# Optimization experiments

Hardware: AMD Instinct MI355X
Metric: run time of the kernel (lower is better)

## Reference

```python
import jax, jax.numpy as jnp
import numpy as np

B, H, W, C = 4, 64, 64, 512
D = C // 8  # query/key channels

def setup_inputs() -> dict:
    key = jax.random.key(0)
    k1, k2, k3, k4, k5 = jax.random.split(key, 5)
    x = jax.random.normal(k1, (B, H, W, C), dtype=jnp.float32)
    # 1x1 convs without bias == per-pixel matmuls; he_normal-ish scaling
    Wq = jax.random.normal(k2, (C, D), dtype=jnp.float32) * np.sqrt(2.0 / C)
    Wk = jax.random.normal(k3, (C, D), dtype=jnp.float32) * np.sqrt(2.0 / C)
    Wv = jax.random.normal(k4, (C, C), dtype=jnp.float32) * np.sqrt(2.0 / C)
    # original init is zeros; use small nonzero so the attention path is exercised
    gamma = jax.random.normal(k5, (1,), dtype=jnp.float32) * 0.1
    return {"x": x, "Wq": Wq, "Wk": Wk, "Wv": Wv, "gamma": gamma}

def reference(x, Wq, Wk, Wv, gamma):
    b, h, w, c = x.shape
    n = h * w
    xf = x.reshape(b, n, c)                      # flatten spatial dims
    q = xf @ Wq                                  # [b, n, c//8]
    k = xf @ Wk                                  # [b, n, c//8]
    v = xf @ Wv                                  # [b, n, c]
    scores = jnp.einsum('bnd,bmd->bnm', q, k)    # [b, n, n]
    attn = jax.nn.sigmoid(scores)                # activation_func='sigmoid' (no row normalization)
    attended = jnp.einsum('bnm,bmc->bnc', attn, v).reshape(b, h, w, c)
    return gamma * attended + x
```

## Files before the change

### kernel.cpp

```cpp
#include <hip/hip_runtime.h>

typedef short bf16x8 __attribute__((ext_vector_type(8)));
typedef float f32x4 __attribute__((ext_vector_type(4)));
typedef unsigned short ushort8v __attribute__((ext_vector_type(8)));
typedef unsigned short ushort4v __attribute__((ext_vector_type(4)));

__device__ __forceinline__ unsigned short f2bf(float f) {
  unsigned u = __float_as_uint(f);
  u += 0x7FFF + ((u >> 16) & 1);
  return (unsigned short)(u >> 16);
}

__global__ void wt_prep(const float* __restrict__ Wq, const float* __restrict__ Wk,
                        const float* __restrict__ Wv, unsigned short* __restrict__ WbT) {
  int idx = blockIdx.x * 256 + threadIdx.x;
  int o = idx >> 9, c = idx & 511;
  float v;
  if (o < 64)       v = Wq[c * 64 + o] * 1.44269504f;
  else if (o < 128) v = Wk[c * 64 + (o - 64)];
  else              v = Wv[(size_t)c * 512 + (o - 128)];
  WbT[idx] = f2bf(v);
}

__global__ __launch_bounds__(256, 2) void proj_gemm(
    const float* __restrict__ x, const unsigned short* __restrict__ WbT,
    unsigned short* __restrict__ q, unsigned short* __restrict__ k,
    unsigned short* __restrict__ vT) {
  __shared__ unsigned short As[128][72];
  const int tid = threadIdx.x;
  const int wid = tid >> 6, lane = tid & 63;
  const int l15 = lane & 15, l4 = lane >> 4;
  const int mtile = blockIdx.x, ntile = blockIdx.y;
  const int rbase = mtile * 128;
  const int wr = (wid >> 1) * 64, wc = (wid & 1) * 64;

  f32x4 acc[4][4] = {};

  const int arow = tid >> 2;
  const int akof = (tid & 3) * 16;

  for (int kb = 0; kb < 512; kb += 64) {
    f32x4 t0[2][4];
#pragma unroll
    for (int pass = 0; pass < 2; ++pass) {
      const float* src = x + (size_t)(rbase + pass * 64 + arow) * 512 + kb + akof;
#pragma unroll
      for (int i = 0; i < 4; ++i) t0[pass][i] = *(const f32x4*)(src + i * 4);
    }
    __syncthreads();
#pragma unroll
    for (int pass = 0; pass < 2; ++pass) {
      unsigned short tmp[16];
#pragma unroll
      for (int i = 0; i < 4; ++i)
#pragma unroll
        for (int j = 0; j < 4; ++j) tmp[i * 4 + j] = f2bf(t0[pass][i][j]);
      unsigned short* dst = &As[pass * 64 + arow][akof];
      *(ushort8v*)(dst)     = *(ushort8v*)(tmp);
      *(ushort8v*)(dst + 8) = *(ushort8v*)(tmp + 8);
    }
    __syncthreads();

    bf16x8 af[4][2], bfr[4][2];
#pragma unroll
    for (int mr = 0; mr < 4; ++mr)
#pragma unroll
      for (int ks = 0; ks < 2; ++ks)
        af[mr][ks] = *(const bf16x8*)&As[wr + mr * 16 + l15][ks * 32 + l4 * 8];
#pragma unroll
    for (int nc = 0; nc < 4; ++nc)
#pragma unroll
      for (int ks = 0; ks < 2; ++ks) {
        int col = ntile * 128 + wc + nc * 16 + l15;
        bfr[nc][ks] = *(const bf16x8*)(WbT + (size_t)col * 512 + kb + ks * 32 + l4 * 8);
      }
#pragma unroll
    for (int ks = 0; ks < 2; ++ks)
#pragma unroll
      for (int mr = 0; mr < 4; ++mr)
#pragma unroll
        for (int nc = 0; nc < 4; ++nc)
          acc[mr][nc] = __builtin_amdgcn_mfma_f32_16x16x32_bf16(af[mr][ks], bfr[nc][ks],
                                                                acc[mr][nc], 0, 0, 0);
  }

  if (ntile == 0) {
    unsigned short* dst = (wid & 1) ? k : q;
#pragma unroll
    for (int mr = 0; mr < 4; ++mr)
#pragma unroll
      for (int nc = 0; nc < 4; ++nc)
#pragma unroll
        for (int r = 0; r < 4; ++r) {
          int grow = rbase + wr + mr * 16 + l4 * 4 + r;
          int col = nc * 16 + l15;
          dst[(size_t)grow * 64 + col] = f2bf(acc[mr][nc][r]);
        }
  } else {
#pragma unroll
    for (int mr = 0; mr < 4; ++mr)
#pragma unroll
      for (int nc = 0; nc < 4; ++nc) {
        int col = ntile * 128 + wc + nc * 16 + l15 - 128;
        int grow = rbase + wr + mr * 16 + l4 * 4;
        int b = grow >> 12, m = grow & 4095;
        ushort4v pk;
#pragma unroll
        for (int r = 0; r < 4; ++r) pk[r] = f2bf(acc[mr][nc][r]);
        *(ushort4v*)(vT + ((size_t)b * 512 + col) * 4096 + m) = pk;
      }
  }
}

__global__ __launch_bounds__(512, 1) void attn_fused(
    const float* __restrict__ x, const unsigned short* __restrict__ q,
    const unsigned short* __restrict__ k, const unsigned short* __restrict__ vT,
    const float* __restrict__ gamma, float* __restrict__ out) {
  __shared__ unsigned short Vs[2][16][8][16][8];
  __shared__ unsigned short Ps[2][8][8][16][8];
  const int tid = threadIdx.x, w = tid >> 6, lane = tid & 63;
  const int l15 = lane & 15, l4 = lane >> 4;
  const int rhalf = w >> 2;
  const int mt = w & 3;
  const int pvt = w >> 1;
  const int ms = w & 1;
  const int rt = blockIdx.x, ct = blockIdx.y, b = blockIdx.z;
  const int rbase = rt * 128, cbase = ct * 256;
  const unsigned short* qb = q + (size_t)b * 4096 * 64;
  const unsigned short* kp = k + (size_t)b * 4096 * 64;
  const unsigned short* vb = vT + (size_t)b * 512 * 4096;
  const float gv = gamma[0];
  const int vst_c = tid >> 1, vhalf = tid & 1;

  bf16x8 qf[4][2];
#pragma unroll
  for (int rf = 0; rf < 4; ++rf)
#pragma unroll
    for (int ks = 0; ks < 2; ++ks)
      qf[rf][ks] = *(const bf16x8*)(qb +
          (size_t)(rbase + rhalf * 64 + rf * 16 + l15) * 64 + ks * 32 + l4 * 8);

  bf16x8 kfc[2];
#pragma unroll
  for (int ks = 0; ks < 2; ++ks)
    kfc[ks] = *(const bf16x8*)(kp + (size_t)(mt * 16 + l15) * 64 + ks * 32 + l4 * 8);
  {
    bf16x8 vv[4];
#pragma unroll
    for (int i = 0; i < 4; ++i)
      vv[i] = *(const bf16x8*)(vb + (size_t)(cbase + vst_c) * 4096 + vhalf * 32 + i * 8);
#pragma unroll
    for (int i = 0; i < 4; ++i)
      *(bf16x8*)&Vs[0][vst_c >> 4][vhalf * 4 + i][vst_c & 15][0] = vv[i];
  }

  f32x4 oacc[8][4] = {};

  for (int it = 0; it < 64; ++it) {
    const int mb_n = (it + 1) * 64;
    const bool pf = (it < 63);
    const int p = it & 1;
    bf16x8 kfn[2], vv[4];
    if (pf) {
#pragma unroll
      for (int ks = 0; ks < 2; ++ks)
        kfn[ks] = *(const bf16x8*)(kp + (size_t)(mb_n + mt * 16 + l15) * 64 + ks * 32 + l4 * 8);
#pragma unroll
      for (int i = 0; i < 4; ++i)
        vv[i] = *(const bf16x8*)(vb + (size_t)(cbase + vst_c) * 4096 + mb_n + vhalf * 32 + i * 8);
    }

    f32x4 sacc[4] = {};
#pragma unroll
    for (int ks = 0; ks < 2; ++ks)
#pragma unroll
      for (int rf = 0; rf < 4; ++rf)
        sacc[rf] = __builtin_amdgcn_mfma_f32_16x16x32_bf16(kfc[ks], qf[rf][ks], sacc[rf], 0, 0, 0);

#pragma unroll
    for (int rf = 0; rf < 4; ++rf) {
      ushort4v pk;
#pragma unroll
      for (int r = 0; r < 4; ++r) {
        float s = sacc[rf][r];
        pk[r] = f2bf(__builtin_amdgcn_rcpf(1.0f + __builtin_amdgcn_exp2f(-s)));
      }
      *(ushort4v*)&Ps[p][rhalf * 4 + rf][mt * 2 + (l4 >> 1)][l15][(l4 & 1) * 4] = pk;
    }
    __syncthreads();

    __builtin_amdgcn_s_setprio(1);
    {
      bf16x8 af[8], bfr[4];
#pragma unroll
      for (int mr = 0; mr < 8; ++mr)
        af[mr] = *(const bf16x8*)&Ps[p][mr][ms * 4 + l4][l15][0];
#pragma unroll
      for (int nc = 0; nc < 4; ++nc)
        bfr[nc] = *(const bf16x8*)&Vs[p][pvt * 4 + nc][ms * 4 + l4][l15][0];
#pragma unroll
      for (int mr = 0; mr < 8; ++mr)
#pragma unroll
        for (int nc = 0; nc < 4; ++nc)
          oacc[mr][nc] = __builtin_amdgcn_mfma_f32_16x16x32_bf16(af[mr], bfr[nc],
                                                                 oacc[mr][nc], 0, 0, 0);
    }
    __builtin_amdgcn_s_setprio(0);

    if (pf) {
#pragma unroll
      for (int i = 0; i < 4; ++i)
        *(bf16x8*)&Vs[p ^ 1][vst_c >> 4][vhalf * 4 + i][vst_c & 15][0] = vv[i];
      kfc[0] = kfn[0]; kfc[1] = kfn[1];
    }
  }

  float* red = (float*)&Vs[0][0][0][0][0];
  __syncthreads();
#pragma unroll
  for (int h = 0; h < 2; ++h) {
    if (ms == 1) {
#pragma unroll
      for (int m4 = 0; m4 < 4; ++m4)
#pragma unroll
        for (int nc = 0; nc < 4; ++nc)
#pragma unroll
          for (int r = 0; r < 4; ++r)
            red[(pvt * 64 + m4 * 16 + l4 * 4 + r) * 64 + nc * 16 + l15] =
                oacc[h * 4 + m4][nc][r];
    }
    __syncthreads();
    if (ms == 0) {
#pragma unroll
      for (int m4 = 0; m4 < 4; ++m4)
#pragma unroll
        for (int nc = 0; nc < 4; ++nc)
#pragma unroll
          for (int r = 0; r < 4; ++r) {
            int mr = h * 4 + m4;
            float sum = oacc[mr][nc][r] +
                red[(pvt * 64 + m4 * 16 + l4 * 4 + r) * 64 + nc * 16 + l15];
            int grow = rbase + mr * 16 + l4 * 4 + r;
            int col = cbase + pvt * 64 + nc * 16 + l15;
            size_t idx = ((size_t)b * 4096 + grow) * 512 + col;
            out[idx] = gv * sum + x[idx];
          }
    }
    __syncthreads();
  }
}

extern "C" void kernel_launch(void* const* d_in, const int* in_sizes, int n_in,
                              void* d_out, int out_size, void* d_ws, size_t ws_size,
                              hipStream_t stream) {
  const float* x     = (const float*)d_in[0];
  const float* Wq    = (const float*)d_in[1];
  const float* Wk    = (const float*)d_in[2];
  const float* Wv    = (const float*)d_in[3];
  const float* gamma = (const float*)d_in[4];
  float* out = (float*)d_out;

  char* ws = (char*)d_ws;
  unsigned short* qbuf = (unsigned short*)(ws);
  unsigned short* kbuf = (unsigned short*)(ws + (2ull << 20));
  unsigned short* vT   = (unsigned short*)(ws + (4ull << 20));
  unsigned short* WbT  = (unsigned short*)(ws + (20ull << 20));

  hipLaunchKernelGGL(wt_prep, dim3(1280), dim3(256), 0, stream, Wq, Wk, Wv, WbT);
  hipLaunchKernelGGL(proj_gemm, dim3(128, 5), dim3(256), 0, stream, x, WbT, qbuf, kbuf, vT);
  hipLaunchKernelGGL(attn_fused, dim3(32, 2, 4), dim3(512), 0, stream,
                     x, qbuf, kbuf, vT, gamma, out);
}
```

Before: 142.2 us.

## Software-pipeline QK scores one tile ahead of the PV matmul

```diff
diff --git a/kernel.cpp b/kernel.cpp
--- a/kernel.cpp
+++ b/kernel.cpp
@@ -140,10 +140,6 @@
       qf[rf][ks] = *(const bf16x8*)(qb +
           (size_t)(rbase + rhalf * 64 + rf * 16 + l15) * 64 + ks * 32 + l4 * 8);
 
-  bf16x8 kfc[2];
-#pragma unroll
-  for (int ks = 0; ks < 2; ++ks)
-    kfc[ks] = *(const bf16x8*)(kp + (size_t)(mt * 16 + l15) * 64 + ks * 32 + l4 * 8);
   {
     bf16x8 vv[4];
 #pragma unroll
@@ -152,42 +148,57 @@
 #pragma unroll
     for (int i = 0; i < 4; ++i)
       *(bf16x8*)&Vs[0][vst_c >> 4][vhalf * 4 + i][vst_c & 15][0] = vv[i];
-  }
+
+    bf16x8 k0[2];
+#pragma unroll
+    for (int ks = 0; ks < 2; ++ks)
+      k0[ks] = *(const bf16x8*)(kp + (size_t)(mt * 16 + l15) * 64 + ks * 32 + l4 * 8);
+    f32x4 s0[4] = {};
+#pragma unroll
+    for (int ks = 0; ks < 2; ++ks)
+#pragma unroll
+      for (int rf = 0; rf < 4; ++rf)
+        s0[rf] = __builtin_amdgcn_mfma_f32_16x16x32_bf16(k0[ks], qf[rf][ks], s0[rf], 0, 0, 0);
+#pragma unroll
+    for (int rf = 0; rf < 4; ++rf) {
+      ushort4v pk;
+#pragma unroll
+      for (int r = 0; r < 4; ++r)
+        pk[r] = f2bf(__builtin_amdgcn_rcpf(1.0f + __builtin_amdgcn_exp2f(-s0[rf][r])));
+      *(ushort4v*)&Ps[0][rhalf * 4 + rf][mt * 2 + (l4 >> 1)][l15][(l4 & 1) * 4] = pk;
+    }
+  }
+  bf16x8 kfc[2];
+#pragma unroll
+  for (int ks = 0; ks < 2; ++ks)
+    kfc[ks] = *(const bf16x8*)(kp + (size_t)(64 + mt * 16 + l15) * 64 + ks * 32 + l4 * 8);
+  __syncthreads();
 
   f32x4 oacc[8][4] = {};
 
   for (int it = 0; it < 64; ++it) {
-    const int mb_n = (it + 1) * 64;
     const bool pf = (it < 63);
     const int p = it & 1;
+    const int kn = (it + 2 < 64) ? (it + 2) : 63;
     bf16x8 kfn[2], vv[4];
+    f32x4 sacc[4] = {};
+
     if (pf) {
 #pragma unroll
+      for (int i = 0; i < 4; ++i)
+        vv[i] = *(const bf16x8*)(vb + (size_t)(cbase + vst_c) * 4096 +
+                                 (it + 1) * 64 + vhalf * 32 + i * 8);
+#pragma unroll
       for (int ks = 0; ks < 2; ++ks)
-        kfn[ks] = *(const bf16x8*)(kp + (size_t)(mb_n + mt * 16 + l15) * 64 + ks * 32 + l4 * 8);
-#pragma unroll
-      for (int i = 0; i < 4; ++i)
-        vv[i] = *(const bf16x8*)(vb + (size_t)(cbase + vst_c) * 4096 + mb_n + vhalf * 32 + i * 8);
-    }
-
-    f32x4 sacc[4] = {};
-#pragma unroll
-    for (int ks = 0; ks < 2; ++ks)
-#pragma unroll
-      for (int rf = 0; rf < 4; ++rf)
-        sacc[rf] = __builtin_amdgcn_mfma_f32_16x16x32_bf16(kfc[ks], qf[rf][ks], sacc[rf], 0, 0, 0);
-
-#pragma unroll
-    for (int rf = 0; rf < 4; ++rf) {
-      ushort4v pk;
-#pragma unroll
-      for (int r = 0; r < 4; ++r) {
-        float s = sacc[rf][r];
-        pk[r] = f2bf(__builtin_amdgcn_rcpf(1.0f + __builtin_amdgcn_exp2f(-s)));
-      }
-      *(ushort4v*)&Ps[p][rhalf * 4 + rf][mt * 2 + (l4 >> 1)][l15][(l4 & 1) * 4] = pk;
-    }
-    __syncthreads();
+        kfn[ks] = *(const bf16x8*)(kp + (size_t)(kn * 64 + mt * 16 + l15) * 64 +
+                                   ks * 32 + l4 * 8);
+#pragma unroll
+      for (int ks = 0; ks < 2; ++ks)
+#pragma unroll
+        for (int rf = 0; rf < 4; ++rf)
+          sacc[rf] = __builtin_amdgcn_mfma_f32_16x16x32_bf16(kfc[ks], qf[rf][ks],
+                                                             sacc[rf], 0, 0, 0);
+    }
 
     __builtin_amdgcn_s_setprio(1);
     {
@@ -209,10 +220,19 @@
 
     if (pf) {
 #pragma unroll
+      for (int rf = 0; rf < 4; ++rf) {
+        ushort4v pk;
+#pragma unroll
+        for (int r = 0; r < 4; ++r)
+          pk[r] = f2bf(__builtin_amdgcn_rcpf(1.0f + __builtin_amdgcn_exp2f(-sacc[rf][r])));
+        *(ushort4v*)&Ps[p ^ 1][rhalf * 4 + rf][mt * 2 + (l4 >> 1)][l15][(l4 & 1) * 4] = pk;
+      }
+#pragma unroll
       for (int i = 0; i < 4; ++i)
         *(bf16x8*)&Vs[p ^ 1][vst_c >> 4][vhalf * 4 + i][vst_c & 15][0] = vv[i];
       kfc[0] = kfn[0]; kfc[1] = kfn[1];
     }
+    __syncthreads();
   }
 
   float* red = (float*)&Vs[0][0][0][0][0];
```

New measurement: 147.0 us. 1.03x slower.
